# Kernel optimization log

Measured on AMD Instinct MI355X. Metric: run time of the kernel, lower is better.

## Reference

```python
import jax, jax.numpy as jnp
import numpy as np

F = 20  # hard-coded feature width in the module


def setup_inputs() -> dict:
    key = jax.random.key(0)
    k1, k2, k3, k4 = jax.random.split(key, 4)
    N = 1048576
    x = jax.random.normal(k1, (N, F), dtype=jnp.float32)
    # nn.Linear(20, 20): weight [out, in], bias [out]
    W = jax.random.normal(k2, (F, F), dtype=jnp.float32) * (1.0 / np.sqrt(F))
    b = jax.random.normal(k3, (F,), dtype=jnp.float32) * 0.01
    rand_weight = jax.random.normal(k4, (F, F), dtype=jnp.float32)
    return {"x": x, "W": W, "b": b, "rand_weight": rand_weight}


def _halving_count(s):
    """Smallest int k >= 0 with s * 2^-k <= 1 (== number of `x /= 2` loop iters)."""
    k = jnp.ceil(jnp.log2(jnp.maximum(s, 1.0))).astype(jnp.int32)
    # guard against float rounding in log2
    k = jnp.where(s * jnp.exp2(-k.astype(jnp.float32)) > 1.0, k + 1, k)
    k = jnp.where((k > 0) & (s * jnp.exp2(-(k - 1).astype(jnp.float32)) <= 1.0), k - 1, k)
    return k


def reference(x, W, b, rand_weight):
    # x = self.linear(x)
    h = x @ W.T + b
    # x = relu(x @ rand_weight + 1)
    h = jax.nn.relu(h @ rand_weight + 1.0)
    # x = self.linear(x)  (shared weights)
    h = h @ W.T + b
    # while x.abs().sum() > 1: x /= 2   ->  x * 2^-k
    s = jnp.sum(jnp.abs(h))
    k = _halving_count(s)
    h = h * jnp.exp2(-k.astype(h.dtype))
    return jnp.sum(h)
```

## Files before the change

kernel.cpp:

```cpp
#include <hip/hip_runtime.h>
#include <math.h>

#define FF 20
#define TPB 256
#define TILES_PER_WAVE 16
#define BT 4

typedef __fp16 half2v __attribute__((ext_vector_type(2)));
typedef __fp16 half8 __attribute__((ext_vector_type(8)));
typedef float f32x4 __attribute__((ext_vector_type(4)));

__global__ void mlp_setup(const float* __restrict__ W, const float* __restrict__ b,
                          const float* __restrict__ R, __fp16* __restrict__ frag) {
    int t = threadIdx.x;
    int f = t >> 6, l = t & 63;
    int g = l >> 4, p = l & 15;
    int row = (f & 1) * 16 + p;
    #pragma unroll
    for (int e = 0; e < 8; ++e) {
        int k = (e < 4) ? (4 * g + e) : (16 + 4 * g + (e - 4));
        float v = 0.f;
        if (f < 2) {
            if (row < FF) {
                if (k < FF) {
                    float s = 0.f;
                    for (int j = 0; j < FF; ++j) s = fmaf(W[j * FF + k], R[j * FF + row], s);
                    v = s;
                } else if (k == FF) {
                    float s = 1.0f;
                    for (int j = 0; j < FF; ++j) s = fmaf(b[j], R[j * FF + row], s);
                    v = s;
                }
            }
        } else {
            if (row < FF) {
                if (k < FF) v = W[row * FF + k];
                else if (k == FF) v = b[row];
            }
        }
        frag[t * 8 + e] = (__fp16)v;
    }
}

__global__ __launch_bounds__(TPB) void mlp_main(
    const float* __restrict__ x, const __fp16* __restrict__ frag,
    double2* __restrict__ partials, int nrows, int ntiles)
{
    const int t = threadIdx.x;
    const int l = t & 63;
    const int g = l >> 4;
    const int r = l & 15;

    const half8 A10 = *reinterpret_cast<const half8*>(frag + (0 * 64 + l) * 8);
    const half8 A11 = *reinterpret_cast<const half8*>(frag + (1 * 64 + l) * 8);
    const half8 A20 = *reinterpret_cast<const half8*>(frag + (2 * 64 + l) * 8);
    const half8 A21 = *reinterpret_cast<const half8*>(frag + (3 * 64 + l) * 8);

    const int wave_id = blockIdx.x * (TPB / 64) + (t >> 6);
    const long tile0 = (long)wave_id * TILES_PER_WAVE;

    float psum = 0.f, pabs = 0.f;
    const f32x4 zero = {0.f, 0.f, 0.f, 0.f};

    for (int bt = 0; bt < TILES_PER_WAVE / BT; ++bt) {
        float4 xa[BT], xb[BT];
        #pragma unroll
        for (int u = 0; u < BT; ++u) {
            long tile = tile0 + bt * BT + u;
            xa[u] = make_float4(0.f, 0.f, 0.f, 0.f);
            xb[u] = make_float4(0.f, 0.f, 0.f, 0.f);
            if (tile < ntiles) {
                long row = tile * 16 + r;
                if (row < nrows) {
                    const float* rowp = x + row * FF;
                    xa[u] = *reinterpret_cast<const float4*>(rowp + 4 * g);
                    if (g == 0)
                        xb[u] = *reinterpret_cast<const float4*>(rowp + 16);
                }
            }
        }
        #pragma unroll
        for (int u = 0; u < BT; ++u) {
            long tile = tile0 + bt * BT + u;
            half8 B1;
            half2v p0 = __builtin_amdgcn_cvt_pkrtz(xa[u].x, xa[u].y);
            half2v p1 = __builtin_amdgcn_cvt_pkrtz(xa[u].z, xa[u].w);
            B1[0] = p0[0]; B1[1] = p0[1]; B1[2] = p1[0]; B1[3] = p1[1];
            if (g == 0) {
                half2v p2 = __builtin_amdgcn_cvt_pkrtz(xb[u].x, xb[u].y);
                half2v p3 = __builtin_amdgcn_cvt_pkrtz(xb[u].z, xb[u].w);
                B1[4] = p2[0]; B1[5] = p2[1]; B1[6] = p3[0]; B1[7] = p3[1];
            } else if (g == 1) {
                B1[4] = (__fp16)1.0f;
                B1[5] = (__fp16)0.f; B1[6] = (__fp16)0.f; B1[7] = (__fp16)0.f;
            } else {
                B1[4] = (__fp16)0.f; B1[5] = (__fp16)0.f;
                B1[6] = (__fp16)0.f; B1[7] = (__fp16)0.f;
            }
            f32x4 c0 = __builtin_amdgcn_mfma_f32_16x16x32_f16(A10, B1, zero, 0, 0, 0);
            f32x4 c1 = __builtin_amdgcn_mfma_f32_16x16x32_f16(A11, B1, zero, 0, 0, 0);
            half8 B2;
            half2v q0 = __builtin_amdgcn_cvt_pkrtz(fmaxf(c0[0], 0.f), fmaxf(c0[1], 0.f));
            half2v q1 = __builtin_amdgcn_cvt_pkrtz(fmaxf(c0[2], 0.f), fmaxf(c0[3], 0.f));
            half2v q2 = __builtin_amdgcn_cvt_pkrtz(fmaxf(c1[0], 0.f), fmaxf(c1[1], 0.f));
            half2v q3 = __builtin_amdgcn_cvt_pkrtz(fmaxf(c1[2], 0.f), fmaxf(c1[3], 0.f));
            B2[0] = q0[0]; B2[1] = q0[1]; B2[2] = q1[0]; B2[3] = q1[1];
            B2[4] = q2[0]; B2[5] = q2[1]; B2[6] = q3[0]; B2[7] = q3[1];
            if (g == 1) B2[4] = (__fp16)1.0f;
            f32x4 d0 = __builtin_amdgcn_mfma_f32_16x16x32_f16(A20, B2, zero, 0, 0, 0);
            f32x4 d1 = __builtin_amdgcn_mfma_f32_16x16x32_f16(A21, B2, zero, 0, 0, 0);
            if (tile * 16 + r < nrows) {
                #pragma unroll
                for (int q = 0; q < 4; ++q) {
                    psum += d0[q];            pabs += fabsf(d0[q]);
                    psum += d1[q];            pabs += fabsf(d1[q]);
                }
            }
        }
    }

    #pragma unroll
    for (int off = 32; off > 0; off >>= 1) {
        psum += __shfl_down(psum, off, 64);
        pabs += __shfl_down(pabs, off, 64);
    }
    __shared__ double wsum[TPB / 64], wabs[TPB / 64];
    if ((t & 63) == 0) { wsum[t >> 6] = (double)psum; wabs[t >> 6] = (double)pabs; }
    __syncthreads();
    if (t == 0) {
        double bs = 0.0, ba = 0.0;
        #pragma unroll
        for (int w = 0; w < TPB / 64; ++w) { bs += wsum[w]; ba += wabs[w]; }
        partials[blockIdx.x] = make_double2(bs, ba);
    }
}

__global__ __launch_bounds__(256) void mlp_final(const double2* __restrict__ parts,
                                                 int nparts, float* __restrict__ out) {
    __shared__ double s_sum[256], s_abs[256];
    int t = threadIdx.x;
    double a = 0.0, sg = 0.0;
    for (int i = t; i < nparts; i += 256) { sg += parts[i].x; a += parts[i].y; }
    s_sum[t] = sg; s_abs[t] = a;
    __syncthreads();
    for (int off = 128; off > 0; off >>= 1) {
        if (t < off) { s_sum[t] += s_sum[t + off]; s_abs[t] += s_abs[t + off]; }
        __syncthreads();
    }
    if (t == 0) {
        double s = s_abs[0];
        int k = 0;
        while (s > 1.0 && k < 4000) { s *= 0.5; ++k; }
        out[0] = (float)ldexp(s_sum[0], -k);
    }
}

extern "C" void kernel_launch(void* const* d_in, const int* in_sizes, int n_in,
                              void* d_out, int out_size, void* d_ws, size_t ws_size,
                              hipStream_t stream) {
    const float* x = (const float*)d_in[0];
    const float* W = (const float*)d_in[1];
    const float* b = (const float*)d_in[2];
    const float* R = (const float*)d_in[3];
    float* out = (float*)d_out;

    __fp16* frag = (__fp16*)d_ws;
    double2* partials = (double2*)((char*)d_ws + 8192);

    int nrows = in_sizes[0] / FF;
    int ntiles = (nrows + 15) / 16;
    int waves = (ntiles + TILES_PER_WAVE - 1) / TILES_PER_WAVE;
    int blocks = (waves + (TPB / 64) - 1) / (TPB / 64);

    hipLaunchKernelGGL(mlp_setup, dim3(1), dim3(256), 0, stream, W, b, R, frag);
    hipLaunchKernelGGL(mlp_main, dim3(blocks), dim3(TPB), 0, stream,
                       x, frag, partials, nrows, ntiles);
    hipLaunchKernelGGL(mlp_final, dim3(1), dim3(256), 0, stream, partials, blocks, out);
}
```

Before: 29.17 us.

## Fuse setup, main and final reduction into one kernel with last-block reduce

```diff
diff --git a/kernel.cpp b/kernel.cpp
--- a/kernel.cpp
+++ b/kernel.cpp
@@ -4,57 +4,62 @@
 #define FF 20
 #define TPB 256
 #define TILES_PER_WAVE 16
-#define BT 4
+#define BT 2
+#define NB (TILES_PER_WAVE / BT)
 
 typedef __fp16 half2v __attribute__((ext_vector_type(2)));
 typedef __fp16 half8 __attribute__((ext_vector_type(8)));
 typedef float f32x4 __attribute__((ext_vector_type(4)));
 
-__global__ void mlp_setup(const float* __restrict__ W, const float* __restrict__ b,
-                          const float* __restrict__ R, __fp16* __restrict__ frag) {
-    int t = threadIdx.x;
-    int f = t >> 6, l = t & 63;
-    int g = l >> 4, p = l & 15;
-    int row = (f & 1) * 16 + p;
-    #pragma unroll
-    for (int e = 0; e < 8; ++e) {
-        int k = (e < 4) ? (4 * g + e) : (16 + 4 * g + (e - 4));
-        float v = 0.f;
-        if (f < 2) {
-            if (row < FF) {
-                if (k < FF) {
-                    float s = 0.f;
-                    for (int j = 0; j < FF; ++j) s = fmaf(W[j * FF + k], R[j * FF + row], s);
-                    v = s;
-                } else if (k == FF) {
-                    float s = 1.0f;
-                    for (int j = 0; j < FF; ++j) s = fmaf(b[j], R[j * FF + row], s);
-                    v = s;
-                }
-            }
-        } else {
-            if (row < FF) {
-                if (k < FF) v = W[row * FF + k];
-                else if (k == FF) v = b[row];
-            }
-        }
-        frag[t * 8 + e] = (__fp16)v;
-    }
-}
-
-__global__ __launch_bounds__(TPB) void mlp_main(
-    const float* __restrict__ x, const __fp16* __restrict__ frag,
-    double2* __restrict__ partials, int nrows, int ntiles)
+__global__ __launch_bounds__(TPB) void mlp_fused(
+    const float* __restrict__ x, const float* __restrict__ W,
+    const float* __restrict__ b, const float* __restrict__ R,
+    unsigned int* __restrict__ counter, double2* __restrict__ partials,
+    float* __restrict__ out, int nrows, int ntiles, int nblocks)
 {
     const int t = threadIdx.x;
     const int l = t & 63;
     const int g = l >> 4;
     const int r = l & 15;
 
-    const half8 A10 = *reinterpret_cast<const half8*>(frag + (0 * 64 + l) * 8);
-    const half8 A11 = *reinterpret_cast<const half8*>(frag + (1 * 64 + l) * 8);
-    const half8 A20 = *reinterpret_cast<const half8*>(frag + (2 * 64 + l) * 8);
-    const half8 A21 = *reinterpret_cast<const half8*>(frag + (3 * 64 + l) * 8);
+    __shared__ float sW[FF * FF], sR[FF * FF], sb[FF];
+    __shared__ float sAt[FF * (FF + 1)];
+    for (int u = t; u < FF * FF; u += TPB) { sW[u] = W[u]; sR[u] = R[u]; }
+    if (t < FF) sb[t] = b[t];
+    __syncthreads();
+    for (int idx = t; idx < FF * (FF + 1); idx += TPB) {
+        int m = idx / (FF + 1), i = idx % (FF + 1);
+        float s;
+        if (i < FF) {
+            s = 0.f;
+            #pragma unroll
+            for (int j = 0; j < FF; ++j) s = fmaf(sW[j * FF + i], sR[j * FF + m], s);
+        } else {
+            s = 1.0f;
+            #pragma unroll
+            for (int j = 0; j < FF; ++j) s = fmaf(sb[j], sR[j * FF + m], s);
+        }
+        sAt[idx] = s;
+    }
+    __syncthreads();
+
+    half8 A10, A11, A20, A21;
+    #pragma unroll
+    for (int e = 0; e < 8; ++e) {
+        int k = (e < 4) ? (4 * g + e) : (16 + 4 * g + (e - 4));
+        int row0 = r, row1 = 16 + r;
+        float v10 = (k <= FF) ? sAt[row0 * (FF + 1) + k] : 0.f;
+        float v11 = (row1 < FF && k <= FF) ? sAt[row1 * (FF + 1) + k] : 0.f;
+        float v20 = 0.f, v21 = 0.f;
+        if (k < FF) v20 = sW[row0 * FF + k];
+        else if (k == FF) v20 = sb[row0];
+        if (row1 < FF) {
+            if (k < FF) v21 = sW[row1 * FF + k];
+            else if (k == FF) v21 = sb[row1];
+        }
+        A10[e] = (__fp16)v10; A11[e] = (__fp16)v11;
+        A20[e] = (__fp16)v20; A21[e] = (__fp16)v21;
+    }
 
     const int wave_id = blockIdx.x * (TPB / 64) + (t >> 6);
     const long tile0 = (long)wave_id * TILES_PER_WAVE;
@@ -62,8 +67,9 @@
     float psum = 0.f, pabs = 0.f;
     const f32x4 zero = {0.f, 0.f, 0.f, 0.f};
 
-    for (int bt = 0; bt < TILES_PER_WAVE / BT; ++bt) {
-        float4 xa[BT], xb[BT];
+    float4 xa_c[BT], xb_c[BT], xa_n[BT], xb_n[BT];
+
+    auto loadb = [&](int bt, float4* xa, float4* xb) {
         #pragma unroll
         for (int u = 0; u < BT; ++u) {
             long tile = tile0 + bt * BT + u;
@@ -79,6 +85,9 @@
                 }
             }
         }
+    };
+
+    auto computeb = [&](int bt, const float4* xa, const float4* xb) {
         #pragma unroll
         for (int u = 0; u < BT; ++u) {
             long tile = tile0 + bt * BT + u;
@@ -117,6 +126,17 @@
                 }
             }
         }
+    };
+
+    loadb(0, xa_c, xb_c);
+    #pragma unroll
+    for (int bt = 0; bt < NB; ++bt) {
+        if (bt + 1 < NB) loadb(bt + 1, xa_n, xb_n);
+        computeb(bt, xa_c, xb_c);
+        if (bt + 1 < NB) {
+            #pragma unroll
+            for (int u = 0; u < BT; ++u) { xa_c[u] = xa_n[u]; xb_c[u] = xb_n[u]; }
+        }
     }
 
     #pragma unroll
@@ -125,6 +145,7 @@
         pabs += __shfl_down(pabs, off, 64);
     }
     __shared__ double wsum[TPB / 64], wabs[TPB / 64];
+    __shared__ int isLast;
     if ((t & 63) == 0) { wsum[t >> 6] = (double)psum; wabs[t >> 6] = (double)pabs; }
     __syncthreads();
     if (t == 0) {
@@ -132,26 +153,34 @@
         #pragma unroll
         for (int w = 0; w < TPB / 64; ++w) { bs += wsum[w]; ba += wabs[w]; }
         partials[blockIdx.x] = make_double2(bs, ba);
-    }
-}
-
-__global__ __launch_bounds__(256) void mlp_final(const double2* __restrict__ parts,
-                                                 int nparts, float* __restrict__ out) {
-    __shared__ double s_sum[256], s_abs[256];
-    int t = threadIdx.x;
-    double a = 0.0, sg = 0.0;
-    for (int i = t; i < nparts; i += 256) { sg += parts[i].x; a += parts[i].y; }
-    s_sum[t] = sg; s_abs[t] = a;
-    __syncthreads();
-    for (int off = 128; off > 0; off >>= 1) {
-        if (t < off) { s_sum[t] += s_sum[t + off]; s_abs[t] += s_abs[t + off]; }
+        __threadfence();
+        unsigned int old = atomicAdd(counter, 1u);
+        isLast = (old == (unsigned int)(nblocks - 1)) ? 1 : 0;
+    }
+    __syncthreads();
+    if (isLast) {
+        __threadfence();
+        __shared__ double s_sum[TPB], s_abs[TPB];
+        double sg = 0.0, a = 0.0;
+        for (int i = t; i < nblocks; i += TPB) {
+            double px = __hip_atomic_load(&partials[i].x, __ATOMIC_RELAXED,
+                                          __HIP_MEMORY_SCOPE_AGENT);
+            double py = __hip_atomic_load(&partials[i].y, __ATOMIC_RELAXED,
+                                          __HIP_MEMORY_SCOPE_AGENT);
+            sg += px; a += py;
+        }
+        s_sum[t] = sg; s_abs[t] = a;
         __syncthreads();
-    }
-    if (t == 0) {
-        double s = s_abs[0];
-        int k = 0;
-        while (s > 1.0 && k < 4000) { s *= 0.5; ++k; }
-        out[0] = (float)ldexp(s_sum[0], -k);
+        for (int off = TPB / 2; off > 0; off >>= 1) {
+            if (t < off) { s_sum[t] += s_sum[t + off]; s_abs[t] += s_abs[t + off]; }
+            __syncthreads();
+        }
+        if (t == 0) {
+            double s = s_abs[0];
+            int k = 0;
+            while (s > 1.0 && k < 4000) { s *= 0.5; ++k; }
+            out[0] = (float)ldexp(s_sum[0], -k);
+        }
     }
 }
 
@@ -164,16 +193,15 @@
     const float* R = (const float*)d_in[3];
     float* out = (float*)d_out;
 
-    __fp16* frag = (__fp16*)d_ws;
-    double2* partials = (double2*)((char*)d_ws + 8192);
+    unsigned int* counter = (unsigned int*)d_ws;
+    double2* partials = (double2*)((char*)d_ws + 256);
 
     int nrows = in_sizes[0] / FF;
     int ntiles = (nrows + 15) / 16;
     int waves = (ntiles + TILES_PER_WAVE - 1) / TILES_PER_WAVE;
     int blocks = (waves + (TPB / 64) - 1) / (TPB / 64);
 
-    hipLaunchKernelGGL(mlp_setup, dim3(1), dim3(256), 0, stream, W, b, R, frag);
-    hipLaunchKernelGGL(mlp_main, dim3(blocks), dim3(TPB), 0, stream,
-                       x, frag, partials, nrows, ntiles);
-    hipLaunchKernelGGL(mlp_final, dim3(1), dim3(256), 0, stream, partials, blocks, out);
+    hipMemsetAsync(d_ws, 0, 256, stream);
+    hipLaunchKernelGGL(mlp_fused, dim3(blocks), dim3(TPB), 0, stream,
+                       x, W, b, R, counter, partials, out, nrows, ntiles, blocks);
 }
```

Measured after the change: 58.41 us. 100% more time.

## Issue all row loads per wave upfront with fewer tiles per wave

Applied to the files above, without the earlier changes.

```diff
diff --git a/kernel.cpp b/kernel.cpp
--- a/kernel.cpp
+++ b/kernel.cpp
@@ -3,8 +3,7 @@
 
 #define FF 20
 #define TPB 256
-#define TILES_PER_WAVE 16
-#define BT 4
+#define TPW 8
 
 typedef __fp16 half2v __attribute__((ext_vector_type(2)));
 typedef __fp16 half8 __attribute__((ext_vector_type(8)));
@@ -57,64 +56,62 @@
     const half8 A21 = *reinterpret_cast<const half8*>(frag + (3 * 64 + l) * 8);
 
     const int wave_id = blockIdx.x * (TPB / 64) + (t >> 6);
-    const long tile0 = (long)wave_id * TILES_PER_WAVE;
+    const int base_row = wave_id * (TPW * 16) + r;
+
+    float4 xa[TPW], xb[TPW];
+    const float* rowp = x + (size_t)base_row * FF;
+    #pragma unroll
+    for (int u = 0; u < TPW; ++u) {
+        int row = base_row + u * 16;
+        xa[u] = make_float4(0.f, 0.f, 0.f, 0.f);
+        if (row < nrows)
+            xa[u] = *reinterpret_cast<const float4*>(rowp + (size_t)u * 16 * FF + 4 * g);
+    }
+    #pragma unroll
+    for (int u = 0; u < TPW; ++u) {
+        int row = base_row + u * 16;
+        xb[u] = make_float4(0.f, 0.f, 0.f, 0.f);
+        if (g == 0 && row < nrows)
+            xb[u] = *reinterpret_cast<const float4*>(rowp + (size_t)u * 16 * FF + 16);
+    }
 
     float psum = 0.f, pabs = 0.f;
     const f32x4 zero = {0.f, 0.f, 0.f, 0.f};
 
-    for (int bt = 0; bt < TILES_PER_WAVE / BT; ++bt) {
-        float4 xa[BT], xb[BT];
-        #pragma unroll
-        for (int u = 0; u < BT; ++u) {
-            long tile = tile0 + bt * BT + u;
-            xa[u] = make_float4(0.f, 0.f, 0.f, 0.f);
-            xb[u] = make_float4(0.f, 0.f, 0.f, 0.f);
-            if (tile < ntiles) {
-                long row = tile * 16 + r;
-                if (row < nrows) {
-                    const float* rowp = x + row * FF;
-                    xa[u] = *reinterpret_cast<const float4*>(rowp + 4 * g);
-                    if (g == 0)
-                        xb[u] = *reinterpret_cast<const float4*>(rowp + 16);
-                }
-            }
+    #pragma unroll
+    for (int u = 0; u < TPW; ++u) {
+        half8 B1;
+        half2v p0 = __builtin_amdgcn_cvt_pkrtz(xa[u].x, xa[u].y);
+        half2v p1 = __builtin_amdgcn_cvt_pkrtz(xa[u].z, xa[u].w);
+        B1[0] = p0[0]; B1[1] = p0[1]; B1[2] = p1[0]; B1[3] = p1[1];
+        if (g == 0) {
+            half2v p2 = __builtin_amdgcn_cvt_pkrtz(xb[u].x, xb[u].y);
+            half2v p3 = __builtin_amdgcn_cvt_pkrtz(xb[u].z, xb[u].w);
+            B1[4] = p2[0]; B1[5] = p2[1]; B1[6] = p3[0]; B1[7] = p3[1];
+        } else if (g == 1) {
+            B1[4] = (__fp16)1.0f;
+            B1[5] = (__fp16)0.f; B1[6] = (__fp16)0.f; B1[7] = (__fp16)0.f;
+        } else {
+            B1[4] = (__fp16)0.f; B1[5] = (__fp16)0.f;
+            B1[6] = (__fp16)0.f; B1[7] = (__fp16)0.f;
         }
-        #pragma unroll
-        for (int u = 0; u < BT; ++u) {
-            long tile = tile0 + bt * BT + u;
-            half8 B1;
-            half2v p0 = __builtin_amdgcn_cvt_pkrtz(xa[u].x, xa[u].y);
-            half2v p1 = __builtin_amdgcn_cvt_pkrtz(xa[u].z, xa[u].w);
-            B1[0] = p0[0]; B1[1] = p0[1]; B1[2] = p1[0]; B1[3] = p1[1];
-            if (g == 0) {
-                half2v p2 = __builtin_amdgcn_cvt_pkrtz(xb[u].x, xb[u].y);
-                half2v p3 = __builtin_amdgcn_cvt_pkrtz(xb[u].z, xb[u].w);
-                B1[4] = p2[0]; B1[5] = p2[1]; B1[6] = p3[0]; B1[7] = p3[1];
-            } else if (g == 1) {
-                B1[4] = (__fp16)1.0f;
-                B1[5] = (__fp16)0.f; B1[6] = (__fp16)0.f; B1[7] = (__fp16)0.f;
-            } else {
-                B1[4] = (__fp16)0.f; B1[5] = (__fp16)0.f;
-                B1[6] = (__fp16)0.f; B1[7] = (__fp16)0.f;
-            }
-            f32x4 c0 = __builtin_amdgcn_mfma_f32_16x16x32_f16(A10, B1, zero, 0, 0, 0);
-            f32x4 c1 = __builtin_amdgcn_mfma_f32_16x16x32_f16(A11, B1, zero, 0, 0, 0);
-            half8 B2;
-            half2v q0 = __builtin_amdgcn_cvt_pkrtz(fmaxf(c0[0], 0.f), fmaxf(c0[1], 0.f));
-            half2v q1 = __builtin_amdgcn_cvt_pkrtz(fmaxf(c0[2], 0.f), fmaxf(c0[3], 0.f));
-            half2v q2 = __builtin_amdgcn_cvt_pkrtz(fmaxf(c1[0], 0.f), fmaxf(c1[1], 0.f));
-            half2v q3 = __builtin_amdgcn_cvt_pkrtz(fmaxf(c1[2], 0.f), fmaxf(c1[3], 0.f));
-            B2[0] = q0[0]; B2[1] = q0[1]; B2[2] = q1[0]; B2[3] = q1[1];
-            B2[4] = q2[0]; B2[5] = q2[1]; B2[6] = q3[0]; B2[7] = q3[1];
-            if (g == 1) B2[4] = (__fp16)1.0f;
-            f32x4 d0 = __builtin_amdgcn_mfma_f32_16x16x32_f16(A20, B2, zero, 0, 0, 0);
-            f32x4 d1 = __builtin_amdgcn_mfma_f32_16x16x32_f16(A21, B2, zero, 0, 0, 0);
-            if (tile * 16 + r < nrows) {
-                #pragma unroll
-                for (int q = 0; q < 4; ++q) {
-                    psum += d0[q];            pabs += fabsf(d0[q]);
-                    psum += d1[q];            pabs += fabsf(d1[q]);
-                }
+        f32x4 c0 = __builtin_amdgcn_mfma_f32_16x16x32_f16(A10, B1, zero, 0, 0, 0);
+        f32x4 c1 = __builtin_amdgcn_mfma_f32_16x16x32_f16(A11, B1, zero, 0, 0, 0);
+        half8 B2;
+        half2v q0 = __builtin_amdgcn_cvt_pkrtz(fmaxf(c0[0], 0.f), fmaxf(c0[1], 0.f));
+        half2v q1 = __builtin_amdgcn_cvt_pkrtz(fmaxf(c0[2], 0.f), fmaxf(c0[3], 0.f));
+        half2v q2 = __builtin_amdgcn_cvt_pkrtz(fmaxf(c1[0], 0.f), fmaxf(c1[1], 0.f));
+        half2v q3 = __builtin_amdgcn_cvt_pkrtz(fmaxf(c1[2], 0.f), fmaxf(c1[3], 0.f));
+        B2[0] = q0[0]; B2[1] = q0[1]; B2[2] = q1[0]; B2[3] = q1[1];
+        B2[4] = q2[0]; B2[5] = q2[1]; B2[6] = q3[0]; B2[7] = q3[1];
+        if (g == 1) B2[4] = (__fp16)1.0f;
+        f32x4 d0 = __builtin_amdgcn_mfma_f32_16x16x32_f16(A20, B2, zero, 0, 0, 0);
+        f32x4 d1 = __builtin_amdgcn_mfma_f32_16x16x32_f16(A21, B2, zero, 0, 0, 0);
+        if (base_row + u * 16 < nrows) {
+            #pragma unroll
+            for (int q = 0; q < 4; ++q) {
+                psum += d0[q];            pabs += fabsf(d0[q]);
+                psum += d1[q];            pabs += fabsf(d1[q]);
             }
         }
     }
@@ -169,7 +166,7 @@
 
     int nrows = in_sizes[0] / FF;
     int ntiles = (nrows + 15) / 16;
-    int waves = (ntiles + TILES_PER_WAVE - 1) / TILES_PER_WAVE;
+    int waves = (ntiles + TPW - 1) / TPW;
     int blocks = (waves + (TPB / 64) - 1) / (TPB / 64);
 
     hipLaunchKernelGGL(mlp_setup, dim3(1), dim3(256), 0, stream, W, b, R, frag);
```

Measured after the change: 30.76 us. +5.4%, slower.
